# Optimization experiments

Hardware: AMD Instinct MI355X
Metric: run time of the kernel (lower is better)

Reference implementation:

```python
import jax, jax.numpy as jnp
import numpy as np

N_NODES = 100000
N_EDGES = 1600000
D = 128


def setup_inputs() -> dict:
    key = jax.random.key(0)
    k1, k2, k3, k4, k5 = jax.random.split(key, 5)
    scale = 1.0 / np.sqrt(D)
    return {
        "x": jax.random.normal(k1, (N_NODES, D), dtype=jnp.float32),
        "edge_index": jax.random.randint(k2, (2, N_EDGES), 0, N_NODES, dtype=jnp.int64),
        "edge_attr": jax.random.normal(k3, (N_EDGES, D), dtype=jnp.float32),
        "w1": jax.random.normal(k4, (D, D), dtype=jnp.float32) * scale,
        "b1": jnp.zeros((D,), dtype=jnp.float32),
        "w2": jax.random.normal(k5, (D, D), dtype=jnp.float32) * scale,
        "b2": jnp.zeros((D,), dtype=jnp.float32),
    }


def reference(x, edge_index, edge_attr, w1, b1, w2, b2):
    # GINEConv: out = MLP((1+eps)*x + sum_{j->i} ReLU(x_j + e_ij)), eps=0
    src = edge_index[0]  # source node j per edge
    dst = edge_index[1]  # target node i per edge
    msg = jax.nn.relu(x[src] + edge_attr)            # [E, D] edge-wise gather + relu
    agg = jax.ops.segment_sum(msg, dst, num_segments=N_NODES)  # [N, D] scatter-sum
    h = x + agg                                      # (1 + eps)*x with eps = 0
    h = jax.nn.relu(h @ w1 + b1)                     # Linear -> ReLU
    return h @ w2 + b2                               # Linear
```

## Files before the change

kernel.cpp:

```cpp
#include <hip/hip_runtime.h>
#include <stdint.h>

#define N_NODES 100000
#define N_EDGES 1600000
#define D 128
#define ROWS_PAD 100096

typedef long long i64;
typedef __attribute__((ext_vector_type(8))) short bf16x8;
typedef __attribute__((ext_vector_type(4))) float f32x4;
typedef __attribute__((ext_vector_type(4))) float fv4;

__device__ __forceinline__ unsigned short f2bf(float f) {
    union { float f; unsigned u; } v; v.f = f;
    unsigned r = v.u + 0x7fff + ((v.u >> 16) & 1);
    return (unsigned short)(r >> 16);
}

#define SCAN_CHUNK 1024
#define SCAN_THREADS 256
#define N_CHUNKS ((N_NODES + SCAN_CHUNK - 1) / SCAN_CHUNK)

__global__ __launch_bounds__(256) void count_zero_kernel(int* __restrict__ counts)
{
    const int i = blockIdx.x * 256 + threadIdx.x;
    if (i < N_NODES) counts[i] = 0;
}

__global__ __launch_bounds__(256) void hist_kernel(
    const int* __restrict__ dst, int* __restrict__ counts)
{
    const int e = blockIdx.x * 256 + threadIdx.x;
    if (e < N_EDGES) atomicAdd(&counts[dst[e]], 1);
}

__global__ __launch_bounds__(SCAN_THREADS) void scan_pass1(
    const int* __restrict__ counts, int* __restrict__ blockSums)
{
    __shared__ int sdata[SCAN_THREADS];
    const int b = blockIdx.x, t = threadIdx.x;
    const int base = b * SCAN_CHUNK + t * 4;
    int s = 0;
    #pragma unroll
    for (int k = 0; k < 4; ++k) {
        const int i = base + k;
        if (i < N_NODES) s += counts[i];
    }
    sdata[t] = s; __syncthreads();
    for (int off = SCAN_THREADS / 2; off > 0; off >>= 1) {
        if (t < off) sdata[t] += sdata[t + off];
        __syncthreads();
    }
    if (t == 0) blockSums[b] = sdata[0];
}

__global__ __launch_bounds__(128) void scan_pass2(
    int* __restrict__ blockSums, int* __restrict__ offsets)
{
    __shared__ int sh[128];
    const int t = threadIdx.x;
    const int v = (t < N_CHUNKS) ? blockSums[t] : 0;
    sh[t] = v; __syncthreads();
    for (int off = 1; off < 128; off <<= 1) {
        const int add = (t >= off) ? sh[t - off] : 0;
        __syncthreads();
        sh[t] += add;
        __syncthreads();
    }
    const int incl = sh[t];
    if (t < N_CHUNKS) blockSums[t] = incl - v;
    if (t == N_CHUNKS - 1) offsets[N_NODES] = incl;
}

__global__ __launch_bounds__(SCAN_THREADS) void scan_pass3(
    const int* __restrict__ counts, const int* __restrict__ blockSums,
    int* __restrict__ offsets, int* __restrict__ cursor)
{
    __shared__ int sh[SCAN_THREADS];
    const int b = blockIdx.x, t = threadIdx.x;
    const int base = b * SCAN_CHUNK + t * 4;
    int v[4]; int s = 0;
    #pragma unroll
    for (int k = 0; k < 4; ++k) {
        const int i = base + k;
        v[k] = (i < N_NODES) ? counts[i] : 0;
        s += v[k];
    }
    sh[t] = s; __syncthreads();
    for (int off = 1; off < SCAN_THREADS; off <<= 1) {
        const int add = (t >= off) ? sh[t - off] : 0;
        __syncthreads();
        sh[t] += add;
        __syncthreads();
    }
    int run = blockSums[b] + (sh[t] - s);
    #pragma unroll
    for (int k = 0; k < 4; ++k) {
        const int i = base + k;
        if (i < N_NODES) { offsets[i] = run; cursor[i] = run; }
        run += v[k];
    }
}

__global__ __launch_bounds__(256) void fill_kernel(
    const int* __restrict__ dst, int* __restrict__ cursor, int* __restrict__ bucket)
{
    const int e = blockIdx.x * 256 + threadIdx.x;
    if (e < N_EDGES) {
        const int pos = atomicAdd(&cursor[dst[e]], 1);
        bucket[pos] = e;
    }
}

__global__ __launch_bounds__(256) void pad_zero_kernel(
    float* __restrict__ h0, unsigned short* __restrict__ h1)
{
    const int i = blockIdx.x * 256 + threadIdx.x;
    const int PADE = (ROWS_PAD - N_NODES) * D;
    if (i < PADE) {
        h0[(i64)N_NODES * D + i] = 0.0f;
        h1[(i64)N_NODES * D + i] = 0;
    }
}

#define PAIR(p) {                                                               \
    const int idx = 2*(p) + half;                                               \
    const bool v = idx < n;                                                     \
    int e_ = __shfl(key, idx);                                                  \
    int s_ = __shfl(sk, idx);                                                   \
    e_ = v ? e_ : 0; s_ = v ? s_ : 0;                                           \
    const fv4 xv = *reinterpret_cast<const fv4*>(x + (i64)s_ * D + c4);         \
    const fv4 ev = __builtin_nontemporal_load(                                  \
        reinterpret_cast<const fv4*>(ea + (i64)e_ * D + c4));                   \
    if (v) {                                                                    \
        acc.x += fmaxf(xv.x + ev.x, 0.f);                                       \
        acc.y += fmaxf(xv.y + ev.y, 0.f);                                       \
        acc.z += fmaxf(xv.z + ev.z, 0.f);                                       \
        acc.w += fmaxf(xv.w + ev.w, 0.f);                                       \
    }                                                                           \
}

__global__ __launch_bounds__(256) void gather_kernel(
    const float* __restrict__ x,
    const int*   __restrict__ srcIdx,
    const float* __restrict__ ea,
    const int*   __restrict__ offsets,
    const int*   __restrict__ bucket,
    float*       __restrict__ h0)
{
    const int wave = threadIdx.x >> 6;
    const int lane = threadIdx.x & 63;
    const int node = blockIdx.x * 4 + wave;
    if (node >= N_NODES) return;
    const int half = lane >> 5;
    const int c4   = (lane & 31) * 4;

    const int p0 = offsets[node];
    const int p1 = offsets[node + 1];

    fv4 acc;
    if (half == 0) acc = *reinterpret_cast<const fv4*>(x + (i64)node * D + c4);
    else           acc = (fv4){0.f, 0.f, 0.f, 0.f};

    for (int base = p0; base < p1; base += 64) {
        const int n = min(64, p1 - base);

        int key = 0x7fffffff;
        if (lane < n) key = bucket[base + lane];

        #pragma unroll
        for (int k = 2; k <= 64; k <<= 1) {
            #pragma unroll
            for (int j = k >> 1; j > 0; j >>= 1) {
                const int other = __shfl_xor(key, j);
                const bool up    = ((lane & k) == 0);
                const bool lower = ((lane & j) == 0);
                key = (lower == up) ? min(key, other) : max(key, other);
            }
        }

        int sk = 0;
        if (lane < n) sk = srcIdx[key];

        const int npair = (n + 1) >> 1;
        int it = 0;
        for (; it + 3 < npair; it += 4) {
            PAIR(it) PAIR(it + 1) PAIR(it + 2) PAIR(it + 3)
        }
        for (; it < npair; ++it) { PAIR(it) }
    }

    acc.x += __shfl_xor(acc.x, 32);
    acc.y += __shfl_xor(acc.y, 32);
    acc.z += __shfl_xor(acc.z, 32);
    acc.w += __shfl_xor(acc.w, 32);

    if (half == 0)
        __builtin_nontemporal_store(acc,
            reinterpret_cast<fv4*>(h0 + (i64)node * D + c4));
}

__global__ __launch_bounds__(256) void mlp1_mfma_kernel(
    const float* __restrict__ hin,
    const float* __restrict__ w,
    const float* __restrict__ bias,
    unsigned short* __restrict__ hout)
{
    const int tid  = threadIdx.x;
    const int wave = tid >> 6;
    const int lane = tid & 63;
    const int g    = lane >> 4;
    const int lr   = lane & 15;
    const int colbase = wave * 32;

    bf16x8 bfrag[4][2];
    #pragma unroll
    for (int ks = 0; ks < 4; ++ks) {
        #pragma unroll
        for (int nt = 0; nt < 2; ++nt) {
            const int col = colbase + nt * 16 + lr;
            const int k0  = ks * 32 + g * 8;
            bf16x8 f;
            #pragma unroll
            for (int j = 0; j < 8; ++j)
                f[j] = (short)f2bf(w[(k0 + j) * D + col]);
            bfrag[ks][nt] = f;
        }
    }
    const float bc0 = bias[colbase + lr];
    const float bc1 = bias[colbase + 16 + lr];

    const int rowbase0 = blockIdx.x * 128;
    #pragma unroll 1
    for (int sub = 0; sub < 8; ++sub) {
        const int rowbase = rowbase0 + sub * 16;
        const int arow = rowbase + lr;

        bf16x8 afrag[4];
        #pragma unroll
        for (int ks = 0; ks < 4; ++ks) {
            const float* ap = hin + (i64)arow * D + ks * 32 + g * 8;
            const float4 u0 = *reinterpret_cast<const float4*>(ap);
            const float4 u1 = *reinterpret_cast<const float4*>(ap + 4);
            bf16x8 f;
            f[0] = (short)f2bf(u0.x); f[1] = (short)f2bf(u0.y);
            f[2] = (short)f2bf(u0.z); f[3] = (short)f2bf(u0.w);
            f[4] = (short)f2bf(u1.x); f[5] = (short)f2bf(u1.y);
            f[6] = (short)f2bf(u1.z); f[7] = (short)f2bf(u1.w);
            afrag[ks] = f;
        }

        f32x4 acc0 = { bc0, bc0, bc0, bc0 };
        f32x4 acc1 = { bc1, bc1, bc1, bc1 };
        #pragma unroll
        for (int ks = 0; ks < 4; ++ks) {
            acc0 = __builtin_amdgcn_mfma_f32_16x16x32_bf16(afrag[ks], bfrag[ks][0], acc0, 0, 0, 0);
            acc1 = __builtin_amdgcn_mfma_f32_16x16x32_bf16(afrag[ks], bfrag[ks][1], acc1, 0, 0, 0);
        }

        #pragma unroll
        for (int r = 0; r < 4; ++r) {
            const int orow = rowbase + g * 4 + r;
            hout[(i64)orow * D + colbase + lr]      = f2bf(fmaxf(acc0[r], 0.f));
            hout[(i64)orow * D + colbase + 16 + lr] = f2bf(fmaxf(acc1[r], 0.f));
        }
    }
}

__global__ __launch_bounds__(256) void mlp2_mfma_kernel(
    const unsigned short* __restrict__ hin,
    const float* __restrict__ w,
    const float* __restrict__ bias,
    float* __restrict__ hout)
{
    const int tid  = threadIdx.x;
    const int wave = tid >> 6;
    const int lane = tid & 63;
    const int g    = lane >> 4;
    const int lr   = lane & 15;
    const int colbase = wave * 32;

    bf16x8 bfrag[4][2];
    #pragma unroll
    for (int ks = 0; ks < 4; ++ks) {
        #pragma unroll
        for (int nt = 0; nt < 2; ++nt) {
            const int col = colbase + nt * 16 + lr;
            const int k0  = ks * 32 + g * 8;
            bf16x8 f;
            #pragma unroll
            for (int j = 0; j < 8; ++j)
                f[j] = (short)f2bf(w[(k0 + j) * D + col]);
            bfrag[ks][nt] = f;
        }
    }
    const float bc0 = bias[colbase + lr];
    const float bc1 = bias[colbase + 16 + lr];

    const int rowbase0 = blockIdx.x * 128;
    #pragma unroll 1
    for (int sub = 0; sub < 8; ++sub) {
        const int rowbase = rowbase0 + sub * 16;
        const int arow = rowbase + lr;

        bf16x8 afrag[4];
        #pragma unroll
        for (int ks = 0; ks < 4; ++ks)
            afrag[ks] = *reinterpret_cast<const bf16x8*>(
                hin + (i64)arow * D + ks * 32 + g * 8);

        f32x4 acc0 = { bc0, bc0, bc0, bc0 };
        f32x4 acc1 = { bc1, bc1, bc1, bc1 };
        #pragma unroll
        for (int ks = 0; ks < 4; ++ks) {
            acc0 = __builtin_amdgcn_mfma_f32_16x16x32_bf16(afrag[ks], bfrag[ks][0], acc0, 0, 0, 0);
            acc1 = __builtin_amdgcn_mfma_f32_16x16x32_bf16(afrag[ks], bfrag[ks][1], acc1, 0, 0, 0);
        }

        #pragma unroll
        for (int r = 0; r < 4; ++r) {
            const int orow = rowbase + g * 4 + r;
            if (orow < N_NODES) {
                hout[(i64)orow * D + colbase + lr]      = acc0[r];
                hout[(i64)orow * D + colbase + 16 + lr] = acc1[r];
            }
        }
    }
}

__global__ __launch_bounds__(256) void init_acc_kernel(
    const float* __restrict__ x, float* __restrict__ acc)
{
    const int i = blockIdx.x * blockDim.x + threadIdx.x;
    const int n = N_NODES * D / 4;
    if (i < n)
        reinterpret_cast<float4*>(acc)[i] = reinterpret_cast<const float4*>(x)[i];
}

__global__ __launch_bounds__(256) void edge_scatter_kernel(
    const float* __restrict__ x,
    const int*  __restrict__ src,
    const int*  __restrict__ dst,
    const float* __restrict__ ea,
    float* __restrict__ acc)
{
    const int lane = threadIdx.x & 31;
    const int grp  = threadIdx.x >> 5;
    const i64 e = (i64)blockIdx.x * 8 + grp;
    if (e >= N_EDGES) return;
    const int s = src[e];
    const int d = dst[e];
    const int j = lane * 4;
    const float4 xv = *reinterpret_cast<const float4*>(x  + (i64)s * D + j);
    const float4 ev = *reinterpret_cast<const float4*>(ea + e * D + j);
    float4 m;
    m.x = fmaxf(xv.x + ev.x, 0.0f);
    m.y = fmaxf(xv.y + ev.y, 0.0f);
    m.z = fmaxf(xv.z + ev.z, 0.0f);
    m.w = fmaxf(xv.w + ev.w, 0.0f);
    float* pp = acc + (i64)d * D + j;
    atomicAdd(pp + 0, m.x);
    atomicAdd(pp + 1, m.y);
    atomicAdd(pp + 2, m.z);
    atomicAdd(pp + 3, m.w);
}

#define MLP_THREADS 512
#define ROWS_PER_CHUNK 16
#define CHUNKS_PER_BLOCK 4
#define ROWS_PER_BLOCK (ROWS_PER_CHUNK * CHUNKS_PER_BLOCK)

template<bool RELU>
__global__ __launch_bounds__(MLP_THREADS) void mlp_layer_kernel(
    const float* __restrict__ hin,
    const float* __restrict__ w,
    const float* __restrict__ b,
    float* __restrict__ hout)
{
    __shared__ float ws_[D * D];
    __shared__ float bs_[D];
    __shared__ float hrow[ROWS_PER_CHUNK][D];

    const int tid = threadIdx.x;
    for (int t = tid; t < D * D / 4; t += MLP_THREADS)
        reinterpret_cast<float4*>(ws_)[t] = reinterpret_cast<const float4*>(w)[t];
    if (tid < D) bs_[tid] = b[tid];

    const int j = tid & (D - 1);
    const int q = tid >> 7;
    const int rowBase = blockIdx.x * ROWS_PER_BLOCK;

    for (int c = 0; c < CHUNKS_PER_BLOCK; ++c) {
        const int chunkRow = rowBase + c * ROWS_PER_CHUNK;
        __syncthreads();
        {
            const int r   = tid >> 5;
            const int col = (tid & 31) * 4;
            const int gi  = chunkRow + r;
            float4 v = make_float4(0.f, 0.f, 0.f, 0.f);
            if (gi < N_NODES)
                v = *reinterpret_cast<const float4*>(hin + (i64)gi * D + col);
            *reinterpret_cast<float4*>(&hrow[r][col]) = v;
        }
        __syncthreads();

        float acc0 = bs_[j], acc1 = bs_[j], acc2 = bs_[j], acc3 = bs_[j];
        const int r0 = q * 4;
        #pragma unroll 4
        for (int k = 0; k < D; ++k) {
            const float wv = ws_[k * D + j];
            acc0 = fmaf(hrow[r0 + 0][k], wv, acc0);
            acc1 = fmaf(hrow[r0 + 1][k], wv, acc1);
            acc2 = fmaf(hrow[r0 + 2][k], wv, acc2);
            acc3 = fmaf(hrow[r0 + 3][k], wv, acc3);
        }
        if (RELU) {
            acc0 = fmaxf(acc0, 0.f); acc1 = fmaxf(acc1, 0.f);
            acc2 = fmaxf(acc2, 0.f); acc3 = fmaxf(acc3, 0.f);
        }
        const int gi = chunkRow + r0;
        if (gi + 0 < N_NODES) hout[(i64)(gi + 0) * D + j] = acc0;
        if (gi + 1 < N_NODES) hout[(i64)(gi + 1) * D + j] = acc1;
        if (gi + 2 < N_NODES) hout[(i64)(gi + 2) * D + j] = acc2;
        if (gi + 3 < N_NODES) hout[(i64)(gi + 3) * D + j] = acc3;
    }
}

extern "C" void kernel_launch(void* const* d_in, const int* in_sizes, int n_in,
                              void* d_out, int out_size, void* d_ws, size_t ws_size,
                              hipStream_t stream)
{
    const float* x  = (const float*)d_in[0];
    const int*   ei = (const int*)  d_in[1];
    const float* ea = (const float*)d_in[2];
    const float* w1 = (const float*)d_in[3];
    const float* b1 = (const float*)d_in[4];
    const float* w2 = (const float*)d_in[5];
    const float* b2 = (const float*)d_in[6];
    float* out = (float*)d_out;

    const int* src = ei;
    const int* dst = ei + N_EDGES;

    const size_t INT_REGION = (size_t)N_NODES + (N_NODES + 1) + N_NODES + 128 + N_EDGES;
    const size_t H_ELEMS    = (size_t)ROWS_PAD * D;
    const size_t WS_NEEDED  = INT_REGION * 4 + 32 + H_ELEMS * 4 + H_ELEMS * 2;

    if (ws_size >= WS_NEEDED) {
        int* counts    = (int*)d_ws;
        int* offsets   = counts + N_NODES;
        int* cursor    = offsets + (N_NODES + 1);
        int* blockSums = cursor + N_NODES;
        int* bucket    = blockSums + 128;
        uintptr_t p = (uintptr_t)(bucket + N_EDGES);
        p = (p + 15) & ~(uintptr_t)15;
        float* h0 = (float*)p;
        unsigned short* h1 = (unsigned short*)(h0 + H_ELEMS);

        count_zero_kernel<<<(N_NODES + 255) / 256, 256, 0, stream>>>(counts);
        hist_kernel<<<(N_EDGES + 255) / 256, 256, 0, stream>>>(dst, counts);
        scan_pass1<<<N_CHUNKS, SCAN_THREADS, 0, stream>>>(counts, blockSums);
        scan_pass2<<<1, 128, 0, stream>>>(blockSums, offsets);
        scan_pass3<<<N_CHUNKS, SCAN_THREADS, 0, stream>>>(counts, blockSums, offsets, cursor);
        fill_kernel<<<(N_EDGES + 255) / 256, 256, 0, stream>>>(dst, cursor, bucket);
        pad_zero_kernel<<<48, 256, 0, stream>>>(h0, h1);
        gather_kernel<<<(N_NODES + 3) / 4, 256, 0, stream>>>(x, src, ea, offsets, bucket, h0);

        const int mlpBlocks = ROWS_PAD / 128;
        mlp1_mfma_kernel<<<mlpBlocks, 256, 0, stream>>>(h0, w1, b1, h1);
        mlp2_mfma_kernel<<<mlpBlocks, 256, 0, stream>>>(h1, w2, b2, out);
    } else {
        const int n = N_NODES * D / 4;
        init_acc_kernel<<<(n + 255) / 256, 256, 0, stream>>>(x, out);
        edge_scatter_kernel<<<(N_EDGES + 7) / 8, 256, 0, stream>>>(x, src, dst, ea, out);
        const int blocks = (N_NODES + ROWS_PER_BLOCK - 1) / ROWS_PER_BLOCK;
        mlp_layer_kernel<true ><<<blocks, MLP_THREADS, 0, stream>>>(out, w1, b1, out);
        mlp_layer_kernel<false><<<blocks, MLP_THREADS, 0, stream>>>(out, w2, b2, out);
    }
}
```

Baseline: 545.2 us.

## Split gather into edge-order bf16 message pass plus CSR segment sum

Replaces the per-node gather, which read edge_attr rows in scattered order after a sort of bucket indices, with an edge-ordered message kernel. That kernel streams edge_attr sequentially, computes relu(x_src+e), and writes bf16 messages into CSR-sorted positions, followed by a per-node segment-sum kernel. The aim is to make the large edge_attr read coalesced and to drop the in-wave bitonic sort. In exchange it adds a 400MB bf16 intermediate write and read, and message precision drops to bf16 before summation.

```diff
diff --git a/kernel.cpp b/kernel.cpp
--- a/kernel.cpp
+++ b/kernel.cpp
@@ -10,11 +10,16 @@
 typedef __attribute__((ext_vector_type(8))) short bf16x8;
 typedef __attribute__((ext_vector_type(4))) float f32x4;
 typedef __attribute__((ext_vector_type(4))) float fv4;
+typedef __attribute__((ext_vector_type(4))) unsigned short usv4;
 
 __device__ __forceinline__ unsigned short f2bf(float f) {
     union { float f; unsigned u; } v; v.f = f;
     unsigned r = v.u + 0x7fff + ((v.u >> 16) & 1);
     return (unsigned short)(r >> 16);
+}
+__device__ __forceinline__ float bf2f(unsigned short h) {
+    union { unsigned u; float f; } v; v.u = ((unsigned)h) << 16;
+    return v.f;
 }
 
 #define SCAN_CHUNK 1024
@@ -102,13 +107,12 @@
     }
 }
 
-__global__ __launch_bounds__(256) void fill_kernel(
-    const int* __restrict__ dst, int* __restrict__ cursor, int* __restrict__ bucket)
+__global__ __launch_bounds__(256) void fill_pos_kernel(
+    const int* __restrict__ dst, int* __restrict__ cursor, int* __restrict__ epos)
 {
     const int e = blockIdx.x * 256 + threadIdx.x;
     if (e < N_EDGES) {
-        const int pos = atomicAdd(&cursor[dst[e]], 1);
-        bucket[pos] = e;
+        epos[e] = atomicAdd(&cursor[dst[e]], 1);
     }
 }
 
@@ -123,81 +127,73 @@
     }
 }
 
-#define PAIR(p) {                                                               \
-    const int idx = 2*(p) + half;                                               \
-    const bool v = idx < n;                                                     \
-    int e_ = __shfl(key, idx);                                                  \
-    int s_ = __shfl(sk, idx);                                                   \
-    e_ = v ? e_ : 0; s_ = v ? s_ : 0;                                           \
-    const fv4 xv = *reinterpret_cast<const fv4*>(x + (i64)s_ * D + c4);         \
-    const fv4 ev = __builtin_nontemporal_load(                                  \
-        reinterpret_cast<const fv4*>(ea + (i64)e_ * D + c4));                   \
-    if (v) {                                                                    \
-        acc.x += fmaxf(xv.x + ev.x, 0.f);                                       \
-        acc.y += fmaxf(xv.y + ev.y, 0.f);                                       \
-        acc.z += fmaxf(xv.z + ev.z, 0.f);                                       \
-        acc.w += fmaxf(xv.w + ev.w, 0.f);                                       \
-    }                                                                           \
-}
-
-__global__ __launch_bounds__(256) void gather_kernel(
+__global__ __launch_bounds__(256) void msg_kernel(
     const float* __restrict__ x,
     const int*   __restrict__ srcIdx,
     const float* __restrict__ ea,
-    const int*   __restrict__ offsets,
-    const int*   __restrict__ bucket,
-    float*       __restrict__ h0)
+    const int*   __restrict__ epos,
+    unsigned short* __restrict__ msgbuf)
+{
+    const int wave = threadIdx.x >> 6;
+    const int lane = threadIdx.x & 63;
+    const int half = lane >> 5;
+    const int c4   = (lane & 31) * 4;
+    const i64 e0 = (i64)blockIdx.x * 32 + wave * 8;
+
+    #pragma unroll
+    for (int k = 0; k < 8; k += 2) {
+        const i64 e = e0 + k + half;
+        const int s   = srcIdx[e];
+        const int pos = epos[e];
+        const fv4 xv = *reinterpret_cast<const fv4*>(x + (i64)s * D + c4);
+        const fv4 ev = __builtin_nontemporal_load(
+            reinterpret_cast<const fv4*>(ea + e * D + c4));
+        usv4 m;
+        m.x = f2bf(fmaxf(xv.x + ev.x, 0.f));
+        m.y = f2bf(fmaxf(xv.y + ev.y, 0.f));
+        m.z = f2bf(fmaxf(xv.z + ev.z, 0.f));
+        m.w = f2bf(fmaxf(xv.w + ev.w, 0.f));
+        __builtin_nontemporal_store(m,
+            reinterpret_cast<usv4*>(msgbuf + (i64)pos * D + c4));
+    }
+}
+
+__global__ __launch_bounds__(256) void segsum_kernel(
+    const float* __restrict__ x,
+    const unsigned short* __restrict__ msgbuf,
+    const int* __restrict__ offsets,
+    float* __restrict__ h0)
 {
     const int wave = threadIdx.x >> 6;
     const int lane = threadIdx.x & 63;
     const int node = blockIdx.x * 4 + wave;
     if (node >= N_NODES) return;
-    const int half = lane >> 5;
-    const int c4   = (lane & 31) * 4;
+    const int c2 = lane * 2;
 
     const int p0 = offsets[node];
     const int p1 = offsets[node + 1];
 
-    fv4 acc;
-    if (half == 0) acc = *reinterpret_cast<const fv4*>(x + (i64)node * D + c4);
-    else           acc = (fv4){0.f, 0.f, 0.f, 0.f};
-
-    for (int base = p0; base < p1; base += 64) {
-        const int n = min(64, p1 - base);
-
-        int key = 0x7fffffff;
-        if (lane < n) key = bucket[base + lane];
-
-        #pragma unroll
-        for (int k = 2; k <= 64; k <<= 1) {
-            #pragma unroll
-            for (int j = k >> 1; j > 0; j >>= 1) {
-                const int other = __shfl_xor(key, j);
-                const bool up    = ((lane & k) == 0);
-                const bool lower = ((lane & j) == 0);
-                key = (lower == up) ? min(key, other) : max(key, other);
-            }
-        }
-
-        int sk = 0;
-        if (lane < n) sk = srcIdx[key];
-
-        const int npair = (n + 1) >> 1;
-        int it = 0;
-        for (; it + 3 < npair; it += 4) {
-            PAIR(it) PAIR(it + 1) PAIR(it + 2) PAIR(it + 3)
-        }
-        for (; it < npair; ++it) { PAIR(it) }
-    }
-
-    acc.x += __shfl_xor(acc.x, 32);
-    acc.y += __shfl_xor(acc.y, 32);
-    acc.z += __shfl_xor(acc.z, 32);
-    acc.w += __shfl_xor(acc.w, 32);
-
-    if (half == 0)
-        __builtin_nontemporal_store(acc,
-            reinterpret_cast<fv4*>(h0 + (i64)node * D + c4));
+    const float2 xv = *reinterpret_cast<const float2*>(x + (i64)node * D + c2);
+    float a0 = xv.x, a1 = xv.y;
+
+    int p = p0;
+    for (; p + 3 < p1; p += 4) {
+        const ushort2 m0 = *reinterpret_cast<const ushort2*>(msgbuf + (i64)(p + 0) * D + c2);
+        const ushort2 m1 = *reinterpret_cast<const ushort2*>(msgbuf + (i64)(p + 1) * D + c2);
+        const ushort2 m2 = *reinterpret_cast<const ushort2*>(msgbuf + (i64)(p + 2) * D + c2);
+        const ushort2 m3 = *reinterpret_cast<const ushort2*>(msgbuf + (i64)(p + 3) * D + c2);
+        a0 += bf2f(m0.x); a1 += bf2f(m0.y);
+        a0 += bf2f(m1.x); a1 += bf2f(m1.y);
+        a0 += bf2f(m2.x); a1 += bf2f(m2.y);
+        a0 += bf2f(m3.x); a1 += bf2f(m3.y);
+    }
+    for (; p < p1; ++p) {
+        const ushort2 m0 = *reinterpret_cast<const ushort2*>(msgbuf + (i64)p * D + c2);
+        a0 += bf2f(m0.x); a1 += bf2f(m0.y);
+    }
+
+    float2 o; o.x = a0; o.y = a1;
+    *reinterpret_cast<float2*>(h0 + (i64)node * D + c2) = o;
 }
 
 __global__ __launch_bounds__(256) void mlp1_mfma_kernel(
@@ -444,27 +440,31 @@
 
     const size_t INT_REGION = (size_t)N_NODES + (N_NODES + 1) + N_NODES + 128 + N_EDGES;
     const size_t H_ELEMS    = (size_t)ROWS_PAD * D;
-    const size_t WS_NEEDED  = INT_REGION * 4 + 32 + H_ELEMS * 4 + H_ELEMS * 2;
+    const size_t MSG_ELEMS  = (size_t)N_EDGES * D;
+    const size_t WS_NEEDED  = INT_REGION * 4 + 128 + H_ELEMS * 4 + H_ELEMS * 2 + MSG_ELEMS * 2;
 
     if (ws_size >= WS_NEEDED) {
         int* counts    = (int*)d_ws;
         int* offsets   = counts + N_NODES;
         int* cursor    = offsets + (N_NODES + 1);
         int* blockSums = cursor + N_NODES;
-        int* bucket    = blockSums + 128;
-        uintptr_t p = (uintptr_t)(bucket + N_EDGES);
-        p = (p + 15) & ~(uintptr_t)15;
+        int* epos      = blockSums + 128;
+        uintptr_t p = (uintptr_t)(epos + N_EDGES);
+        p = (p + 63) & ~(uintptr_t)63;
         float* h0 = (float*)p;
         unsigned short* h1 = (unsigned short*)(h0 + H_ELEMS);
+        unsigned short* msgbuf = h1 + H_ELEMS;
 
         count_zero_kernel<<<(N_NODES + 255) / 256, 256, 0, stream>>>(counts);
         hist_kernel<<<(N_EDGES + 255) / 256, 256, 0, stream>>>(dst, counts);
         scan_pass1<<<N_CHUNKS, SCAN_THREADS, 0, stream>>>(counts, blockSums);
         scan_pass2<<<1, 128, 0, stream>>>(blockSums, offsets);
         scan_pass3<<<N_CHUNKS, SCAN_THREADS, 0, stream>>>(counts, blockSums, offsets, cursor);
-        fill_kernel<<<(N_EDGES + 255) / 256, 256, 0, stream>>>(dst, cursor, bucket);
+        fill_pos_kernel<<<(N_EDGES + 255) / 256, 256, 0, stream>>>(dst, cursor, epos);
         pad_zero_kernel<<<48, 256, 0, stream>>>(h0, h1);
-        gather_kernel<<<(N_NODES + 3) / 4, 256, 0, stream>>>(x, src, ea, offsets, bucket, h0);
+
+        msg_kernel<<<N_EDGES / 32, 256, 0, stream>>>(x, src, ea, epos, msgbuf);
+        segsum_kernel<<<(N_NODES + 3) / 4, 256, 0, stream>>>(x, msgbuf, offsets, h0);
 
         const int mlpBlocks = ROWS_PAD / 128;
         mlp1_mfma_kernel<<<mlpBlocks, 256, 0, stream>>>(h0, w1, b1, h1);
```

Result: slower. 580.6 us (+6.5%).

## Store gathered x and aggregated h0 in bf16 to halve gather traffic

Applied to the files above, without the earlier changes.

Adds a pre-pass that converts x to bf16, so the per-edge gather of source rows reads 2-byte values instead of 4-byte floats. The aggregated h0 is also written in bf16, which lets mlp1 load MFMA A-fragments directly without converting. This cuts random-gather bandwidth and intermediate write/read volume. In exchange it adds a full pass over x and rounds x to bf16 before the edge-wise add and ReLU, which lowers accuracy.

```diff
diff --git a/kernel.cpp b/kernel.cpp
--- a/kernel.cpp
+++ b/kernel.cpp
@@ -10,11 +10,31 @@
 typedef __attribute__((ext_vector_type(8))) short bf16x8;
 typedef __attribute__((ext_vector_type(4))) float f32x4;
 typedef __attribute__((ext_vector_type(4))) float fv4;
+typedef __attribute__((ext_vector_type(4))) unsigned short usv4;
+typedef __attribute__((ext_vector_type(8))) unsigned short usv8;
 
 __device__ __forceinline__ unsigned short f2bf(float f) {
     union { float f; unsigned u; } v; v.f = f;
     unsigned r = v.u + 0x7fff + ((v.u >> 16) & 1);
     return (unsigned short)(r >> 16);
+}
+__device__ __forceinline__ float bf2f(unsigned short h) {
+    union { unsigned u; float f; } v; v.u = ((unsigned)h) << 16;
+    return v.f;
+}
+
+__global__ __launch_bounds__(256) void xcvt_kernel(
+    const float* __restrict__ x, unsigned short* __restrict__ xb)
+{
+    const i64 b = ((i64)blockIdx.x * 256 + threadIdx.x) * 8;
+    if (b < (i64)N_NODES * D) {
+        const fv4 u0 = *reinterpret_cast<const fv4*>(x + b);
+        const fv4 u1 = *reinterpret_cast<const fv4*>(x + b + 4);
+        usv8 o;
+        o.s0 = f2bf(u0.x); o.s1 = f2bf(u0.y); o.s2 = f2bf(u0.z); o.s3 = f2bf(u0.w);
+        o.s4 = f2bf(u1.x); o.s5 = f2bf(u1.y); o.s6 = f2bf(u1.z); o.s7 = f2bf(u1.w);
+        *reinterpret_cast<usv8*>(xb + b) = o;
+    }
 }
 
 #define SCAN_CHUNK 1024
@@ -113,12 +133,12 @@
 }
 
 __global__ __launch_bounds__(256) void pad_zero_kernel(
-    float* __restrict__ h0, unsigned short* __restrict__ h1)
+    unsigned short* __restrict__ h0, unsigned short* __restrict__ h1)
 {
     const int i = blockIdx.x * 256 + threadIdx.x;
     const int PADE = (ROWS_PAD - N_NODES) * D;
     if (i < PADE) {
-        h0[(i64)N_NODES * D + i] = 0.0f;
+        h0[(i64)N_NODES * D + i] = 0;
         h1[(i64)N_NODES * D + i] = 0;
     }
 }
@@ -129,24 +149,25 @@
     int e_ = __shfl(key, idx);                                                  \
     int s_ = __shfl(sk, idx);                                                   \
     e_ = v ? e_ : 0; s_ = v ? s_ : 0;                                           \
-    const fv4 xv = *reinterpret_cast<const fv4*>(x + (i64)s_ * D + c4);         \
+    const usv4 xv = *reinterpret_cast<const usv4*>(xb + (i64)s_ * D + c4);      \
     const fv4 ev = __builtin_nontemporal_load(                                  \
         reinterpret_cast<const fv4*>(ea + (i64)e_ * D + c4));                   \
     if (v) {                                                                    \
-        acc.x += fmaxf(xv.x + ev.x, 0.f);                                       \
-        acc.y += fmaxf(xv.y + ev.y, 0.f);                                       \
-        acc.z += fmaxf(xv.z + ev.z, 0.f);                                       \
-        acc.w += fmaxf(xv.w + ev.w, 0.f);                                       \
+        acc.x += fmaxf(bf2f(xv.x) + ev.x, 0.f);                                 \
+        acc.y += fmaxf(bf2f(xv.y) + ev.y, 0.f);                                 \
+        acc.z += fmaxf(bf2f(xv.z) + ev.z, 0.f);                                 \
+        acc.w += fmaxf(bf2f(xv.w) + ev.w, 0.f);                                 \
     }                                                                           \
 }
 
 __global__ __launch_bounds__(256) void gather_kernel(
     const float* __restrict__ x,
+    const unsigned short* __restrict__ xb,
     const int*   __restrict__ srcIdx,
     const float* __restrict__ ea,
     const int*   __restrict__ offsets,
     const int*   __restrict__ bucket,
-    float*       __restrict__ h0)
+    unsigned short* __restrict__ h0)
 {
     const int wave = threadIdx.x >> 6;
     const int lane = threadIdx.x & 63;
@@ -195,13 +216,16 @@
     acc.z += __shfl_xor(acc.z, 32);
     acc.w += __shfl_xor(acc.w, 32);
 
-    if (half == 0)
-        __builtin_nontemporal_store(acc,
-            reinterpret_cast<fv4*>(h0 + (i64)node * D + c4));
+    if (half == 0) {
+        usv4 o;
+        o.x = f2bf(acc.x); o.y = f2bf(acc.y);
+        o.z = f2bf(acc.z); o.w = f2bf(acc.w);
+        *reinterpret_cast<usv4*>(h0 + (i64)node * D + c4) = o;
+    }
 }
 
 __global__ __launch_bounds__(256) void mlp1_mfma_kernel(
-    const float* __restrict__ hin,
+    const unsigned short* __restrict__ hin,
     const float* __restrict__ w,
     const float* __restrict__ bias,
     unsigned short* __restrict__ hout)
@@ -238,17 +262,9 @@
 
         bf16x8 afrag[4];
         #pragma unroll
-        for (int ks = 0; ks < 4; ++ks) {
-            const float* ap = hin + (i64)arow * D + ks * 32 + g * 8;
-            const float4 u0 = *reinterpret_cast<const float4*>(ap);
-            const float4 u1 = *reinterpret_cast<const float4*>(ap + 4);
-            bf16x8 f;
-            f[0] = (short)f2bf(u0.x); f[1] = (short)f2bf(u0.y);
-            f[2] = (short)f2bf(u0.z); f[3] = (short)f2bf(u0.w);
-            f[4] = (short)f2bf(u1.x); f[5] = (short)f2bf(u1.y);
-            f[6] = (short)f2bf(u1.z); f[7] = (short)f2bf(u1.w);
-            afrag[ks] = f;
-        }
+        for (int ks = 0; ks < 4; ++ks)
+            afrag[ks] = *reinterpret_cast<const bf16x8*>(
+                hin + (i64)arow * D + ks * 32 + g * 8);
 
         f32x4 acc0 = { bc0, bc0, bc0, bc0 };
         f32x4 acc1 = { bc1, bc1, bc1, bc1 };
@@ -443,8 +459,9 @@
     const int* dst = ei + N_EDGES;
 
     const size_t INT_REGION = (size_t)N_NODES + (N_NODES + 1) + N_NODES + 128 + N_EDGES;
+    const size_t X_ELEMS    = (size_t)N_NODES * D;
     const size_t H_ELEMS    = (size_t)ROWS_PAD * D;
-    const size_t WS_NEEDED  = INT_REGION * 4 + 32 + H_ELEMS * 4 + H_ELEMS * 2;
+    const size_t WS_NEEDED  = INT_REGION * 4 + 64 + (X_ELEMS + 2 * H_ELEMS) * 2;
 
     if (ws_size >= WS_NEEDED) {
         int* counts    = (int*)d_ws;
@@ -453,10 +470,12 @@
         int* blockSums = cursor + N_NODES;
         int* bucket    = blockSums + 128;
         uintptr_t p = (uintptr_t)(bucket + N_EDGES);
-        p = (p + 15) & ~(uintptr_t)15;
-        float* h0 = (float*)p;
-        unsigned short* h1 = (unsigned short*)(h0 + H_ELEMS);
-
+        p = (p + 63) & ~(uintptr_t)63;
+        unsigned short* xb = (unsigned short*)p;
+        unsigned short* h0 = xb + X_ELEMS;
+        unsigned short* h1 = h0 + H_ELEMS;
+
+        xcvt_kernel<<<(int)(X_ELEMS / 8 + 255) / 256, 256, 0, stream>>>(x, xb);
         count_zero_kernel<<<(N_NODES + 255) / 256, 256, 0, stream>>>(counts);
         hist_kernel<<<(N_EDGES + 255) / 256, 256, 0, stream>>>(dst, counts);
         scan_pass1<<<N_CHUNKS, SCAN_THREADS, 0, stream>>>(counts, blockSums);
@@ -464,7 +483,7 @@
         scan_pass3<<<N_CHUNKS, SCAN_THREADS, 0, stream>>>(counts, blockSums, offsets, cursor);
         fill_kernel<<<(N_EDGES + 255) / 256, 256, 0, stream>>>(dst, cursor, bucket);
         pad_zero_kernel<<<48, 256, 0, stream>>>(h0, h1);
-        gather_kernel<<<(N_NODES + 3) / 4, 256, 0, stream>>>(x, src, ea, offsets, bucket, h0);
+        gather_kernel<<<(N_NODES + 3) / 4, 256, 0, stream>>>(x, xb, src, ea, offsets, bucket, h0);
 
         const int mlpBlocks = ROWS_PAD / 128;
         mlp1_mfma_kernel<<<mlpBlocks, 256, 0, stream>>>(h0, w1, b1, h1);
```

Measured after the change: 486.7 us. -10.7%, faster.
